# Optimization experiments

Hardware: AMD Instinct MI355X
Metric: run time of the kernel (lower is better)

Reference implementation:

```python
import jax, jax.numpy as jnp
import numpy as np

MARGIN = 0.3
LOSS_FLOOR = 1e-06


def setup_inputs() -> dict:
    key = jax.random.key(0)
    k1, k2 = jax.random.split(key)
    embeddings = jax.random.normal(k1, (8192, 128), dtype=jnp.float32)
    labels = jax.random.randint(k2, (8192,), 0, 512, dtype=jnp.int64)
    return {"embeddings": embeddings, "labels": labels}


def _pairwise_dist(x):
    # Euclidean cdist via the GEMM identity; clamp for numerical safety.
    sq = jnp.sum(x * x, axis=1)  # [N]
    d2 = sq[:, None] + sq[None, :] - 2.0 * (x @ x.T)  # [N, N]
    return jnp.sqrt(jnp.maximum(d2, 1e-12))


def reference(embeddings, labels):
    dist = _pairwise_dist(embeddings)  # [N, N]
    same = labels[None, :] == labels[:, None]  # [N, N]
    n = embeddings.shape[0]
    eye = jnp.eye(n, dtype=bool)
    mask_pos = same & ~eye
    mask_neg = ~same  # diagonal is same-label, so already excluded

    neg_inf = jnp.float32(-jnp.inf)
    pos_inf = jnp.float32(jnp.inf)
    hardest_pos = jnp.max(jnp.where(mask_pos, dist, neg_inf), axis=1)  # [N]
    hardest_neg = jnp.min(jnp.where(mask_neg, dist, pos_inf), axis=1)  # [N]

    valid = jnp.any(mask_pos, axis=1) & jnp.any(mask_neg, axis=1)  # [N]
    per_row = jnp.maximum(hardest_pos - hardest_neg + MARGIN, LOSS_FLOOR)
    num_valid = jnp.sum(valid)
    total = jnp.sum(jnp.where(valid, per_row, 0.0))
    return jnp.where(num_valid > 0, total / jnp.maximum(num_valid, 1), 0.0).astype(embeddings.dtype)
```

## Files before the change

kernel.cpp:

```cpp
#include <hip/hip_runtime.h>
#include <math.h>


#define NROWS 8192
#define DIM   128
#define JSPLIT 32
#define JCHUNK (NROWS / JSPLIT)
#define NSUB   4
#define SUBROWS 64

typedef short bf16x8 __attribute__((ext_vector_type(8)));
typedef float f32x4  __attribute__((ext_vector_type(4)));

static __device__ __forceinline__ unsigned short f2bf(float f) {
    unsigned u = __float_as_uint(f);
    unsigned r = (u + 0x7FFFu + ((u >> 16) & 1u)) >> 16;
    return (unsigned short)r;
}

static __device__ __forceinline__ unsigned encf(float f) {
    unsigned u = __float_as_uint(f);
    return (u & 0x80000000u) ? ~u : (u | 0x80000000u);
}
static __device__ __forceinline__ float decf(unsigned e) {
    unsigned u = (e & 0x80000000u) ? (e & 0x7FFFFFFFu) : ~e;
    return __uint_as_float(u);
}
#define ENC_PINF 0xFF800000u
#define ENC_NINF 0x007FFFFFu

static __device__ __forceinline__ void gload_lds16(const void* g, void* l) {
    __builtin_amdgcn_global_load_lds(
        (const __attribute__((address_space(1))) unsigned int*)g,
        (__attribute__((address_space(3))) unsigned int*)l, 16, 0, 0);
}

__global__ __launch_bounds__(256) void prep_kernel(
    const float* __restrict__ x, const int* __restrict__ labels,
    int* __restrict__ hist, float* __restrict__ sqp,
    float* __restrict__ sqh, unsigned* __restrict__ hpE,
    unsigned* __restrict__ hnE, unsigned short* __restrict__ xb) {
    int t = blockIdx.x * 256 + threadIdx.x;
    int row = t >> 5;
    int c = t & 31;
    float4 v = ((const float4*)x)[t];
    float ps = v.x * v.x + v.y * v.y + v.z * v.z + v.w * v.w;
#pragma unroll
    for (int s = 1; s < 32; s <<= 1) ps += __shfl_xor(ps, s, 64);
    if (c == 0) {
        sqp[row] = ps;
        sqh[row] = -0.5f * ps;
        atomicAdd(&hist[labels[row]], 1);
    } else if (c == 1) {
        hpE[row] = ENC_PINF;
    } else if (c == 2) {
        hnE[row] = ENC_NINF;
    }
    ushort4 ob;
    ob.x = f2bf(v.x); ob.y = f2bf(v.y); ob.z = f2bf(v.z); ob.w = f2bf(v.w);
    ((ushort4*)xb)[t] = ob;
}

__global__ __launch_bounds__(256, 4) void pair_kernel(
    const unsigned short* __restrict__ xb, const float* __restrict__ sqh,
    const int* __restrict__ labels,
    unsigned* __restrict__ hpE, unsigned* __restrict__ hnE) {
    __shared__ __attribute__((aligned(16))) unsigned char abuf[2][SUBROWS * 256];
    __shared__ __attribute__((aligned(16))) float sqs[JCHUNK];
    __shared__ __attribute__((aligned(16))) int labs[JCHUNK];

    const int tid = threadIdx.x;
    const int lane = tid & 63;
    const int wid = tid >> 6;
    const int q = lane >> 4;
    const int r = lane & 15;
    const int ibase = blockIdx.x * 256 + wid * 64;
    const int jbase = blockIdx.y * JCHUNK;

    sqs[tid] = sqh[jbase + tid];
    labs[tid] = labels[jbase + tid];

    bf16x8 bfrag[4][4];
    int labi[4];
#pragma unroll
    for (int sub = 0; sub < 4; ++sub) {
        int irow = ibase + sub * 16 + r;
        labi[sub] = labels[irow];
#pragma unroll
        for (int ks = 0; ks < 4; ++ks)
            bfrag[sub][ks] = *(const bf16x8*)(xb + (size_t)irow * DIM + ks * 32 + q * 8);
    }

    float hp[4] = {INFINITY, INFINITY, INFINITY, INFINITY};
    float hn[4] = {-INFINITY, -INFINITY, -INFINITY, -INFINITY};

    auto stage = [&](int s, int buf) {
        const char* gb = (const char*)xb + (size_t)(jbase + s * SUBROWS) * 256;
        unsigned char* lb = &abuf[buf][0];
#pragma unroll
        for (int p = 0; p < 4; ++p) {
            int row = wid * 16 + p * 4 + (lane >> 4);
            int colb = (lane & 15) * 16;
            const void* g = gb + row * 256 + (colb ^ ((row & 15) << 4));
            void* l = lb + wid * 4096 + p * 1024;
            gload_lds16(g, l);
        }
    };

    auto compute_tile = [&](int s, int buf, int t) {
        const unsigned char* lb = &abuf[buf][0];
        const int tt = s * 4 + t;
        bf16x8 af[4];
        const int rowb = (t * 16 + r) * 256;
        const int sw = r << 4;
#pragma unroll
        for (int ks = 0; ks < 4; ++ks)
            af[ks] = *(const bf16x8*)(lb + rowb + ((ks * 64 + q * 16) ^ sw));
        f32x4 ci = *(const f32x4*)(&sqs[tt * 16 + q * 4]);
        int4 labj = *(const int4*)(labs + tt * 16 + q * 4);
#pragma unroll
        for (int sub = 0; sub < 4; ++sub) {
            f32x4 acc = ci;
            acc = __builtin_amdgcn_mfma_f32_16x16x32_bf16(af[0], bfrag[sub][0], acc, 0, 0, 0);
            acc = __builtin_amdgcn_mfma_f32_16x16x32_bf16(af[1], bfrag[sub][1], acc, 0, 0, 0);
            acc = __builtin_amdgcn_mfma_f32_16x16x32_bf16(af[2], bfrag[sub][2], acc, 0, 0, 0);
            acc = __builtin_amdgcn_mfma_f32_16x16x32_bf16(af[3], bfrag[sub][3], acc, 0, 0, 0);
            const int li = labi[sub];
            float u0 = acc[0], u1 = acc[1], u2 = acc[2], u3 = acc[3];
            hp[sub] = fminf(hp[sub], (labj.x == li) ? u0 : INFINITY);
            hn[sub] = fmaxf(hn[sub], (labj.x == li) ? -INFINITY : u0);
            hp[sub] = fminf(hp[sub], (labj.y == li) ? u1 : INFINITY);
            hn[sub] = fmaxf(hn[sub], (labj.y == li) ? -INFINITY : u1);
            hp[sub] = fminf(hp[sub], (labj.z == li) ? u2 : INFINITY);
            hn[sub] = fmaxf(hn[sub], (labj.z == li) ? -INFINITY : u2);
            hp[sub] = fminf(hp[sub], (labj.w == li) ? u3 : INFINITY);
            hn[sub] = fmaxf(hn[sub], (labj.w == li) ? -INFINITY : u3);
        }
    };

    stage(0, 0);
    __syncthreads();
#pragma unroll
    for (int s = 0; s < NSUB; ++s) {
        if (s + 1 < NSUB) stage(s + 1, (s + 1) & 1);
#pragma unroll
        for (int t = 0; t < 4; ++t) compute_tile(s, s & 1, t);
        __syncthreads();
    }

#pragma unroll
    for (int sub = 0; sub < 4; ++sub) {
        hp[sub] = fminf(hp[sub], __shfl_xor(hp[sub], 16, 64));
        hp[sub] = fminf(hp[sub], __shfl_xor(hp[sub], 32, 64));
        hn[sub] = fmaxf(hn[sub], __shfl_xor(hn[sub], 16, 64));
        hn[sub] = fmaxf(hn[sub], __shfl_xor(hn[sub], 32, 64));
    }
    if (lane < 16) {
#pragma unroll
        for (int sub = 0; sub < 4; ++sub) {
            int irow = ibase + sub * 16 + lane;
            atomicMin(&hpE[irow], encf(hp[sub]));
            atomicMax(&hnE[irow], encf(hn[sub]));
        }
    }
}

__global__ __launch_bounds__(256) void reduce_kernel(
    const unsigned* __restrict__ hpE, const unsigned* __restrict__ hnE,
    const float* __restrict__ sqp, const int* __restrict__ labels,
    const int* __restrict__ hist, float* __restrict__ gsum,
    float* __restrict__ gcnt, unsigned* __restrict__ done,
    float* __restrict__ out) {
    int row = blockIdx.x * 256 + threadIdx.x;
    float mnp = decf(hpE[row]);
    float mxn = decf(hnE[row]);
    float s = sqp[row];
    int h = hist[labels[row]];
    float sum = 0.f, cnt = 0.f;
    if (h >= 2 && h < NROWS) {
        float dp = sqrtf(fmaxf(s - 2.f * mnp, 1e-12f));
        float dn = sqrtf(fmaxf(s - 2.f * mxn, 1e-12f));
        sum = fmaxf(dp - dn + 0.3f, 1e-6f);
        cnt = 1.f;
    }
#pragma unroll
    for (int sh = 1; sh < 64; sh <<= 1) {
        sum += __shfl_xor(sum, sh, 64);
        cnt += __shfl_xor(cnt, sh, 64);
    }
    __shared__ float ss[4], sc[4];
    int w = threadIdx.x >> 6;
    if ((threadIdx.x & 63) == 0) { ss[w] = sum; sc[w] = cnt; }
    __syncthreads();
    if (threadIdx.x == 0) {
        atomicAdd(gsum, ss[0] + ss[1] + ss[2] + ss[3]);
        atomicAdd(gcnt, sc[0] + sc[1] + sc[2] + sc[3]);
        __threadfence();
        unsigned t = atomicAdd(done, 1u);
        if (t == gridDim.x - 1) {
            float S = atomicAdd(gsum, 0.f);
            float C = atomicAdd(gcnt, 0.f);
            out[0] = (C > 0.f) ? S / C : 0.f;
        }
    }
}

extern "C" void kernel_launch(void* const* d_in, const int* in_sizes, int n_in,
                              void* d_out, int out_size, void* d_ws, size_t ws_size,
                              hipStream_t stream) {
    const float* x = (const float*)d_in[0];
    const int* labels = (const int*)d_in[1];
    float* out = (float*)d_out;

    char* ws = (char*)d_ws;
    int* hist = (int*)ws;
    float* gsum = (float*)(ws + 2048);
    float* gcnt = (float*)(ws + 2052);
    unsigned* done = (unsigned*)(ws + 2056);
    float* sqp = (float*)(ws + 4096);
    float* sqh = (float*)(ws + 36864);
    unsigned* hpE = (unsigned*)(ws + 69632);
    unsigned* hnE = (unsigned*)(ws + 102400);
    unsigned short* xb = (unsigned short*)(ws + 135168);

    hipMemsetAsync(ws, 0, 4096, stream);
    prep_kernel<<<(NROWS * 32) / 256, 256, 0, stream>>>(
        x, labels, hist, sqp, sqh, hpE, hnE, xb);
    pair_kernel<<<dim3(NROWS / 256, JSPLIT), 256, 0, stream>>>(
        xb, sqh, labels, hpE, hnE);
    reduce_kernel<<<NROWS / 256, 256, 0, stream>>>(
        hpE, hnE, sqp, labels, hist, gsum, gcnt, done, out);
}
```

Before: 94.56 us.

## Exploit distance symmetry: compute upper-triangular tiles and update both row and column

The pair kernel now computes only upper-triangular 128x128 block pairs (2080 blocks). Off-diagonal tiles feed both the i-row minima/maxima and, through shuffle and LDS atomic reductions, the j-row ones, which roughly halves the MFMA work. The self-pair is excluded explicitly, and validity is read from whether the positive or negative extrema stayed at their sentinel. That removes the label histogram, its memset and the per-row histogram lookups. In exchange each tile does extra shuffles, LDS atomics and more global atomics, and the smaller 128-row tiles give less reuse per block.

```diff
diff --git a/kernel.cpp b/kernel.cpp
--- a/kernel.cpp
+++ b/kernel.cpp
@@ -4,10 +4,11 @@
 
 #define NROWS 8192
 #define DIM   128
-#define JSPLIT 32
-#define JCHUNK (NROWS / JSPLIT)
-#define NSUB   4
+#define NCH   64
+#define CHROWS 128
+#define NSUB  2
 #define SUBROWS 64
+#define NBLK  (NCH * (NCH + 1) / 2)
 
 typedef short bf16x8 __attribute__((ext_vector_type(8)));
 typedef float f32x4  __attribute__((ext_vector_type(4)));
@@ -36,10 +37,11 @@
 }
 
 __global__ __launch_bounds__(256) void prep_kernel(
-    const float* __restrict__ x, const int* __restrict__ labels,
-    int* __restrict__ hist, float* __restrict__ sqp,
+    const float* __restrict__ x, float* __restrict__ sqp,
     float* __restrict__ sqh, unsigned* __restrict__ hpE,
-    unsigned* __restrict__ hnE, unsigned short* __restrict__ xb) {
+    unsigned* __restrict__ hnE, unsigned short* __restrict__ xb,
+    float* __restrict__ gsum, float* __restrict__ gcnt,
+    unsigned* __restrict__ done) {
     int t = blockIdx.x * 256 + threadIdx.x;
     int row = t >> 5;
     int c = t & 31;
@@ -50,11 +52,12 @@
     if (c == 0) {
         sqp[row] = ps;
         sqh[row] = -0.5f * ps;
-        atomicAdd(&hist[labels[row]], 1);
     } else if (c == 1) {
         hpE[row] = ENC_PINF;
     } else if (c == 2) {
         hnE[row] = ENC_NINF;
+    } else if (t == 3) {
+        *gsum = 0.f; *gcnt = 0.f; *done = 0u;
     }
     ushort4 ob;
     ob.x = f2bf(v.x); ob.y = f2bf(v.y); ob.z = f2bf(v.z); ob.w = f2bf(v.w);
@@ -66,33 +69,45 @@
     const int* __restrict__ labels,
     unsigned* __restrict__ hpE, unsigned* __restrict__ hnE) {
     __shared__ __attribute__((aligned(16))) unsigned char abuf[2][SUBROWS * 256];
-    __shared__ __attribute__((aligned(16))) float sqs[JCHUNK];
-    __shared__ __attribute__((aligned(16))) int labs[JCHUNK];
+    __shared__ __attribute__((aligned(16))) float sqs[CHROWS];
+    __shared__ __attribute__((aligned(16))) int labs[CHROWS];
+    __shared__ unsigned jminE[CHROWS], jmaxE[CHROWS];
 
     const int tid = threadIdx.x;
     const int lane = tid & 63;
     const int wid = tid >> 6;
     const int q = lane >> 4;
     const int r = lane & 15;
-    const int ibase = blockIdx.x * 256 + wid * 64;
-    const int jbase = blockIdx.y * JCHUNK;
-
-    sqs[tid] = sqh[jbase + tid];
-    labs[tid] = labels[jbase + tid];
-
-    bf16x8 bfrag[4][4];
-    int labi[4];
-#pragma unroll
-    for (int sub = 0; sub < 4; ++sub) {
+
+    int rem = blockIdx.x, cbi = 0;
+    while (rem >= NCH - cbi) { rem -= NCH - cbi; ++cbi; }
+    const int cbj = cbi + rem;
+    const bool diag = (cbi == cbj);
+    const int ibase = cbi * CHROWS + wid * 32;
+    const int jbase = cbj * CHROWS;
+
+    if (tid < CHROWS) {
+        sqs[tid] = sqh[jbase + tid];
+        labs[tid] = labels[jbase + tid];
+        jminE[tid] = ENC_PINF;
+        jmaxE[tid] = ENC_NINF;
+    }
+
+    bf16x8 bfrag[2][4];
+    int labi[2];
+    float sqhi[2];
+#pragma unroll
+    for (int sub = 0; sub < 2; ++sub) {
         int irow = ibase + sub * 16 + r;
         labi[sub] = labels[irow];
+        sqhi[sub] = sqh[irow];
 #pragma unroll
         for (int ks = 0; ks < 4; ++ks)
             bfrag[sub][ks] = *(const bf16x8*)(xb + (size_t)irow * DIM + ks * 32 + q * 8);
     }
 
-    float hp[4] = {INFINITY, INFINITY, INFINITY, INFINITY};
-    float hn[4] = {-INFINITY, -INFINITY, -INFINITY, -INFINITY};
+    float hp[2] = {INFINITY, INFINITY};
+    float hn[2] = {-INFINITY, -INFINITY};
 
     auto stage = [&](int s, int buf) {
         const char* gb = (const char*)xb + (size_t)(jbase + s * SUBROWS) * 256;
@@ -116,25 +131,63 @@
 #pragma unroll
         for (int ks = 0; ks < 4; ++ks)
             af[ks] = *(const bf16x8*)(lb + rowb + ((ks * 64 + q * 16) ^ sw));
-        f32x4 ci = *(const f32x4*)(&sqs[tt * 16 + q * 4]);
+        f32x4 cin = *(const f32x4*)(&sqs[tt * 16 + q * 4]);
         int4 labj = *(const int4*)(labs + tt * 16 + q * 4);
-#pragma unroll
-        for (int sub = 0; sub < 4; ++sub) {
-            f32x4 acc = ci;
+        const int jg = jbase + tt * 16 + q * 4;
+
+        float jmn[4] = {INFINITY, INFINITY, INFINITY, INFINITY};
+        float jmx[4] = {-INFINITY, -INFINITY, -INFINITY, -INFINITY};
+
+#pragma unroll
+        for (int sub = 0; sub < 2; ++sub) {
+            f32x4 acc = cin;
             acc = __builtin_amdgcn_mfma_f32_16x16x32_bf16(af[0], bfrag[sub][0], acc, 0, 0, 0);
             acc = __builtin_amdgcn_mfma_f32_16x16x32_bf16(af[1], bfrag[sub][1], acc, 0, 0, 0);
             acc = __builtin_amdgcn_mfma_f32_16x16x32_bf16(af[2], bfrag[sub][2], acc, 0, 0, 0);
             acc = __builtin_amdgcn_mfma_f32_16x16x32_bf16(af[3], bfrag[sub][3], acc, 0, 0, 0);
             const int li = labi[sub];
+            const float adj = sqhi[sub];
+            const int irowg = ibase + sub * 16 + r;
             float u0 = acc[0], u1 = acc[1], u2 = acc[2], u3 = acc[3];
-            hp[sub] = fminf(hp[sub], (labj.x == li) ? u0 : INFINITY);
-            hn[sub] = fmaxf(hn[sub], (labj.x == li) ? -INFINITY : u0);
-            hp[sub] = fminf(hp[sub], (labj.y == li) ? u1 : INFINITY);
-            hn[sub] = fmaxf(hn[sub], (labj.y == li) ? -INFINITY : u1);
-            hp[sub] = fminf(hp[sub], (labj.z == li) ? u2 : INFINITY);
-            hn[sub] = fmaxf(hn[sub], (labj.z == li) ? -INFINITY : u2);
-            hp[sub] = fminf(hp[sub], (labj.w == li) ? u3 : INFINITY);
-            hn[sub] = fmaxf(hn[sub], (labj.w == li) ? -INFINITY : u3);
+            bool s0 = (labj.x == li), s1 = (labj.y == li);
+            bool s2 = (labj.z == li), s3 = (labj.w == li);
+            hp[sub] = fminf(hp[sub], (s0 && (jg + 0) != irowg) ? u0 : INFINITY);
+            hp[sub] = fminf(hp[sub], (s1 && (jg + 1) != irowg) ? u1 : INFINITY);
+            hp[sub] = fminf(hp[sub], (s2 && (jg + 2) != irowg) ? u2 : INFINITY);
+            hp[sub] = fminf(hp[sub], (s3 && (jg + 3) != irowg) ? u3 : INFINITY);
+            hn[sub] = fmaxf(hn[sub], s0 ? -INFINITY : u0);
+            hn[sub] = fmaxf(hn[sub], s1 ? -INFINITY : u1);
+            hn[sub] = fmaxf(hn[sub], s2 ? -INFINITY : u2);
+            hn[sub] = fmaxf(hn[sub], s3 ? -INFINITY : u3);
+            if (!diag) {
+                float v0 = u0 - cin[0] + adj, v1 = u1 - cin[1] + adj;
+                float v2 = u2 - cin[2] + adj, v3 = u3 - cin[3] + adj;
+                jmn[0] = fminf(jmn[0], s0 ? v0 : INFINITY);
+                jmn[1] = fminf(jmn[1], s1 ? v1 : INFINITY);
+                jmn[2] = fminf(jmn[2], s2 ? v2 : INFINITY);
+                jmn[3] = fminf(jmn[3], s3 ? v3 : INFINITY);
+                jmx[0] = fmaxf(jmx[0], s0 ? -INFINITY : v0);
+                jmx[1] = fmaxf(jmx[1], s1 ? -INFINITY : v1);
+                jmx[2] = fmaxf(jmx[2], s2 ? -INFINITY : v2);
+                jmx[3] = fmaxf(jmx[3], s3 ? -INFINITY : v3);
+            }
+        }
+        if (!diag) {
+#pragma unroll
+            for (int e = 0; e < 4; ++e) {
+#pragma unroll
+                for (int m = 1; m < 16; m <<= 1) {
+                    jmn[e] = fminf(jmn[e], __shfl_xor(jmn[e], m, 64));
+                    jmx[e] = fmaxf(jmx[e], __shfl_xor(jmx[e], m, 64));
+                }
+            }
+            if (r == 0) {
+#pragma unroll
+                for (int e = 0; e < 4; ++e) {
+                    atomicMin(&jminE[tt * 16 + q * 4 + e], encf(jmn[e]));
+                    atomicMax(&jmaxE[tt * 16 + q * 4 + e], encf(jmx[e]));
+                }
+            }
         }
     };
 
@@ -149,7 +202,7 @@
     }
 
 #pragma unroll
-    for (int sub = 0; sub < 4; ++sub) {
+    for (int sub = 0; sub < 2; ++sub) {
         hp[sub] = fminf(hp[sub], __shfl_xor(hp[sub], 16, 64));
         hp[sub] = fminf(hp[sub], __shfl_xor(hp[sub], 32, 64));
         hn[sub] = fmaxf(hn[sub], __shfl_xor(hn[sub], 16, 64));
@@ -157,29 +210,35 @@
     }
     if (lane < 16) {
 #pragma unroll
-        for (int sub = 0; sub < 4; ++sub) {
+        for (int sub = 0; sub < 2; ++sub) {
             int irow = ibase + sub * 16 + lane;
-            atomicMin(&hpE[irow], encf(hp[sub]));
-            atomicMax(&hnE[irow], encf(hn[sub]));
-        }
+            unsigned ep = encf(hp[sub]);
+            if (ep != ENC_PINF) atomicMin(&hpE[irow], ep);
+            unsigned en = encf(hn[sub]);
+            if (en != ENC_NINF) atomicMax(&hnE[irow], en);
+        }
+    }
+    if (!diag && tid < CHROWS) {
+        unsigned jm = jminE[tid];
+        if (jm != ENC_PINF) atomicMin(&hpE[jbase + tid], jm);
+        unsigned jx = jmaxE[tid];
+        if (jx != ENC_NINF) atomicMax(&hnE[jbase + tid], jx);
     }
 }
 
 __global__ __launch_bounds__(256) void reduce_kernel(
     const unsigned* __restrict__ hpE, const unsigned* __restrict__ hnE,
-    const float* __restrict__ sqp, const int* __restrict__ labels,
-    const int* __restrict__ hist, float* __restrict__ gsum,
+    const float* __restrict__ sqp, float* __restrict__ gsum,
     float* __restrict__ gcnt, unsigned* __restrict__ done,
     float* __restrict__ out) {
     int row = blockIdx.x * 256 + threadIdx.x;
-    float mnp = decf(hpE[row]);
-    float mxn = decf(hnE[row]);
+    unsigned hpv = hpE[row];
+    unsigned hnv = hnE[row];
     float s = sqp[row];
-    int h = hist[labels[row]];
     float sum = 0.f, cnt = 0.f;
-    if (h >= 2 && h < NROWS) {
-        float dp = sqrtf(fmaxf(s - 2.f * mnp, 1e-12f));
-        float dn = sqrtf(fmaxf(s - 2.f * mxn, 1e-12f));
+    if (hpv != ENC_PINF && hnv != ENC_NINF) {
+        float dp = sqrtf(fmaxf(s - 2.f * decf(hpv), 1e-12f));
+        float dn = sqrtf(fmaxf(s - 2.f * decf(hnv), 1e-12f));
         sum = fmaxf(dp - dn + 0.3f, 1e-6f);
         cnt = 1.f;
     }
@@ -213,21 +272,18 @@
     float* out = (float*)d_out;
 
     char* ws = (char*)d_ws;
-    int* hist = (int*)ws;
-    float* gsum = (float*)(ws + 2048);
-    float* gcnt = (float*)(ws + 2052);
-    unsigned* done = (unsigned*)(ws + 2056);
+    float* gsum = (float*)ws;
+    float* gcnt = (float*)(ws + 4);
+    unsigned* done = (unsigned*)(ws + 8);
     float* sqp = (float*)(ws + 4096);
     float* sqh = (float*)(ws + 36864);
     unsigned* hpE = (unsigned*)(ws + 69632);
     unsigned* hnE = (unsigned*)(ws + 102400);
     unsigned short* xb = (unsigned short*)(ws + 135168);
 
-    hipMemsetAsync(ws, 0, 4096, stream);
     prep_kernel<<<(NROWS * 32) / 256, 256, 0, stream>>>(
-        x, labels, hist, sqp, sqh, hpE, hnE, xb);
-    pair_kernel<<<dim3(NROWS / 256, JSPLIT), 256, 0, stream>>>(
-        xb, sqh, labels, hpE, hnE);
+        x, sqp, sqh, hpE, hnE, xb, gsum, gcnt, done);
+    pair_kernel<<<NBLK, 256, 0, stream>>>(xb, sqh, labels, hpE, hnE);
     reduce_kernel<<<NROWS / 256, 256, 0, stream>>>(
-        hpE, hnE, sqp, labels, hist, gsum, gcnt, done, out);
-}
+        hpE, hnE, sqp, gsum, gcnt, done, out);
+}
```

Measured after the change: 119.4 us. +26.3%, slower.
